# Kernel optimization log

Hardware: AMD Instinct MI355X
Metric: run time of the kernel (lower is better)

Reference implementation:

```python
import jax, jax.numpy as jnp
import numpy as np
from jax import lax

EPSILON = 1e-12


def _sobel_kernels(n1=1, n2=2, n3=2):
    Sx = np.asarray([[[-n1, 0, n1], [-n2, 0, n2], [-n1, 0, n1]],
                     [[-n2, 0, n2], [-n3 * n2, 0, n3 * n2], [-n2, 0, n2]],
                     [[-n1, 0, n1], [-n2, 0, n2], [-n1, 0, n1]]])
    Sy = np.asarray([[[-n1, -n2, -n1], [0, 0, 0], [n1, n2, n1]],
                     [[-n2, -n3 * n2, -n2], [0, 0, 0], [n2, n3 * n2, n2]],
                     [[-n1, -n2, -n1], [0, 0, 0], [n1, n2, n1]]])
    Sz = np.asarray([[[-n1, -n2, -n1], [-n2, -n3 * n2, -n2], [-n1, -n2, -n1]],
                     [[0, 0, 0], [0, 0, 0], [0, 0, 0]],
                     [[n1, n2, n1], [n2, n3 * n2, n2], [n1, n2, n1]]])
    Sd11 = np.asarray([[[0, n1, n2], [-n1, 0, n1], [-n2, -n1, 0]],
                       [[0, n2, n2 * n3], [-n2, 0, n2], [-n2 * n3, -n2, 0]],
                       [[0, n1, n2], [-n1, 0, n1], [-n2, -n1, 0]]])
    Sd12 = np.asarray([[[-n2, -n1, 0], [-n1, 0, n1], [0, n1, n2]],
                       [[-n2 * n3, -n2, 0], [-n2, 0, n2], [0, n2, n2 * n3]],
                       [[-n2, -n1, 0], [-n1, 0, n1], [0, n1, n2]]])
    Sd21 = Sd11.T
    Sd22 = Sd12.T
    Sd31 = np.asarray([-S.T for S in Sd11.T])
    Sd32 = np.asarray([S.T for S in Sd12.T])
    ks = np.stack([Sx, Sy, Sz, Sd11, Sd12, Sd21, Sd22, Sd31, Sd32]).astype(np.float32)
    return jnp.asarray(ks[:, None])  # [9, 1, 3, 3, 3] (OIDHW)


_KERNELS = _sobel_kernels(1, 2, 2)


def _edge_magnitude(img):
    # img: [B, C, H, W, D]. Per-channel convs are summed over C in the original;
    # by linearity of conv, sum channels first, then run all 9 stencils at once.
    C = img.shape[1]
    x = jnp.sum(img, axis=1, keepdims=True)  # [B, 1, H, W, D]
    g = lax.conv_general_dilated(
        x, _KERNELS, window_strides=(1, 1, 1), padding='SAME',
        dimension_numbers=('NCDHW', 'OIDHW', 'NCDHW'))  # [B, 9, H, W, D]
    mag = jnp.sqrt(jnp.sum(g * g, axis=1, keepdims=True) + EPSILON)
    return mag / C  # (1/C) * sqrt(sum_sq + eps), matches operator precedence


def setup_inputs() -> dict:
    key = jax.random.key(0)
    k1, k2 = jax.random.split(key)
    shape = (2, 2, 128, 128, 128)
    y = jax.random.normal(k1, shape, dtype=jnp.float32)
    yp = jax.random.normal(k2, shape, dtype=jnp.float32)
    return {"y": y, "yp": yp}


def reference(y, yp):
    y_edge = _edge_magnitude(y)
    yp_edge = _edge_magnitude(yp)
    return jnp.mean((y_edge - yp_edge) ** 2)  # nn.MSELoss default 'mean'
```

## Files before the change

kernel.cpp:

```cpp
#include <hip/hip_runtime.h>


namespace {

constexpr int ZDIM = 128, YDIM = 128, XDIM = 128;
constexpr int TX = 64, TY = 4, ZC = 16;
constexpr int YX = YDIM * XDIM;
constexpr size_t CS = (size_t)ZDIM * YX;
constexpr float INV_N = 1.0f / 4194304.0f;

__device__ __forceinline__ float bperm(int addr, float v) {
  return __int_as_float(__builtin_amdgcn_ds_bpermute(addr, __float_as_int(v)));
}

__device__ __forceinline__ float edge_mag_half(const float* __restrict__ Ca,
                                               const float* __restrict__ Cb,
                                               const float* __restrict__ Cc) {
  const float g1  = __builtin_fmaf(2.0f, Cb[0], Ca[0] + Cc[0]);
  const float g2  = __builtin_fmaf(2.0f, Cb[1], Ca[1] + Cc[1]);
  const float g3  = Cc[2] - Ca[2];
  const float Azx = __builtin_fmaf(2.0f, Cb[3], Ca[3] + Cc[3]);
  const float Azy = __builtin_fmaf(2.0f, Cb[4], Ca[4] + Cc[4]);
  const float Axz = Cc[5] - Ca[5];
  const float Axy = g2 - Cb[1];
  const float Ayx = g1 - Cb[0];
  const float Ayz = Cc[6] - Ca[6];
  const float g4 = Azx - Azy, g5 = Azx + Azy;
  const float g6 = Axz - Axy, g7 = Axz + Axy;
  const float g8 = Ayx - Ayz, g9 = Ayx + Ayz;
  float s = __builtin_fmaf(g1, g1, 1e-12f);
  s = __builtin_fmaf(g2, g2, s); s = __builtin_fmaf(g3, g3, s);
  s = __builtin_fmaf(g4, g4, s); s = __builtin_fmaf(g5, g5, s);
  s = __builtin_fmaf(g6, g6, s); s = __builtin_fmaf(g7, g7, s);
  s = __builtin_fmaf(g8, g8, s); s = __builtin_fmaf(g9, g9, s);
  return 0.5f * sqrtf(s);
}

__global__ __launch_bounds__(256)
void gme_loss_kernel(const float* __restrict__ y,
                     const float* __restrict__ yp,
                     float* __restrict__ out) {
  const int lane = threadIdx.x;
  const int ty   = threadIdx.y;
  const int tid  = ty * TX + lane;

  const int bx = blockIdx.x;
  const int x0 = (bx & 1) * TX;
  const int yy = (bx >> 1) * TY + ty;
  const int z0 = blockIdx.y * ZC;
  const int b  = blockIdx.z;

  const float* Y0 = y  + (size_t)b * 2 * CS;
  const float* Y1 = Y0 + CS;
  const float* P0 = yp + (size_t)b * 2 * CS;
  const float* P1 = P0 + CS;

  const int vox = yy * XDIM + x0 + lane;
  const bool okM0 = (yy > 0);
  const bool okP0 = (yy < YDIM - 1);

  const bool left  = (lane == 0);
  const bool right = (lane == TX - 1);
  const int  hx    = left ? (x0 - 1) : (x0 + TX);
  const bool hok   = (left && x0 > 0) || (right && x0 + TX < XDIM);
  const int  hxc   = hx < 0 ? 0 : (hx > XDIM - 1 ? XDIM - 1 : hx);
  const int  hvox  = yy * XDIM + hxc;

  const int addrL = (lane > 0 ? lane - 1 : 0) << 2;
  const int addrR = (lane < TX - 1 ? lane + 1 : TX - 1) << 2;

  float pr[2][6];
  float hr[2][6];
  float KY[3][7] = {}, KP[3][7] = {};
  float acc = 0.0f;

  auto loadSum = [&](int buf, int zc) {
    const bool zok = (unsigned)zc < (unsigned)ZDIM;
    const int  zca = zok ? zc : 0;
    const int  o   = zca * YX + vox;
    const int  h   = zca * YX + hvox;
    float ym0=0.f,ym1=0.f,pm0=0.f,pm1=0.f,hym0=0.f,hym1=0.f,hpm0=0.f,hpm1=0.f;
    if (zok && okM0) {
      ym0 = Y0[o - XDIM]; ym1 = Y1[o - XDIM];
      pm0 = P0[o - XDIM]; pm1 = P1[o - XDIM];
      hym0 = Y0[h - XDIM]; hym1 = Y1[h - XDIM];
      hpm0 = P0[h - XDIM]; hpm1 = P1[h - XDIM];
    }
    float yc0=0.f,yc1=0.f,pc0=0.f,pc1=0.f,hyc0=0.f,hyc1=0.f,hpc0=0.f,hpc1=0.f;
    if (zok) {
      yc0 = Y0[o]; yc1 = Y1[o]; pc0 = P0[o]; pc1 = P1[o];
      hyc0 = Y0[h]; hyc1 = Y1[h]; hpc0 = P0[h]; hpc1 = P1[h];
    }
    float yq0=0.f,yq1=0.f,pq0=0.f,pq1=0.f,hyq0=0.f,hyq1=0.f,hpq0=0.f,hpq1=0.f;
    if (zok && okP0) {
      yq0 = Y0[o + XDIM]; yq1 = Y1[o + XDIM];
      pq0 = P0[o + XDIM]; pq1 = P1[o + XDIM];
      hyq0 = Y0[h + XDIM]; hyq1 = Y1[h + XDIM];
      hpq0 = P0[h + XDIM]; hpq1 = P1[h + XDIM];
    }
    pr[buf][0] = ym0 + ym1; pr[buf][1] = yc0 + yc1; pr[buf][2] = yq0 + yq1;
    pr[buf][3] = pm0 + pm1; pr[buf][4] = pc0 + pc1; pr[buf][5] = pq0 + pq1;
    hr[buf][0] = hok ? hym0 + hym1 : 0.f;
    hr[buf][1] = hok ? hyc0 + hyc1 : 0.f;
    hr[buf][2] = hok ? hyq0 + hyq1 : 0.f;
    hr[buf][3] = hok ? hpm0 + hpm1 : 0.f;
    hr[buf][4] = hok ? hpc0 + hpc1 : 0.f;
    hr[buf][5] = hok ? hpq0 + hpq1 : 0.f;
  };

  auto volCombos = [&](float rm, float rc, float rp,
                       float hm, float hc, float hp, float* __restrict__ C) {
    const float t   = rm + rp;
    const float ys  = __builtin_fmaf(2.0f, rc, t);
    const float yd  = rp - rm;
    const float ye  = t + rc;
    const float th  = hm + hp;
    const float hys = __builtin_fmaf(2.0f, hc, th);
    const float hyd = hp - hm;
    const float hye = th + hc;
    float ysL = bperm(addrL, ys), ysR = bperm(addrR, ys);
    float ydL = bperm(addrL, yd), ydR = bperm(addrR, yd);
    float yeL = bperm(addrL, ye), yeR = bperm(addrR, ye);
    ysL = left ? hys : ysL;   ysR = right ? hys : ysR;
    ydL = left ? hyd : ydL;   ydR = right ? hyd : ydR;
    yeL = left ? hye : yeL;   yeR = right ? hye : yeR;
    const float tS = ysL + ysR, tD = ydL + ydR, tE = yeL + yeR;
    C[0] = ysR - ysL;
    C[2] = __builtin_fmaf(2.0f, ys, tS);
    C[6] = tS + ys;
    C[1] = __builtin_fmaf(2.0f, yd, tD);
    C[4] = tD + yd;
    C[3] = yeR - yeL;
    C[5] = __builtin_fmaf(2.0f, ye, tE);
  };

  loadSum(0, z0 - 1);

#pragma unroll 6
  for (int j = 0; j < ZC + 2; ++j) {
    const int cur = j & 1;
    if (j < ZC + 1) loadSum(cur ^ 1, z0 + j);

    float* Cy = KY[j % 3];
    float* Cp = KP[j % 3];
    volCombos(pr[cur][0], pr[cur][1], pr[cur][2],
              hr[cur][0], hr[cur][1], hr[cur][2], Cy);
    volCombos(pr[cur][3], pr[cur][4], pr[cur][5],
              hr[cur][3], hr[cur][4], hr[cur][5], Cp);

    if (j >= 2) {
      const float my = edge_mag_half(KY[(j + 1) % 3], KY[(j + 2) % 3], Cy);
      const float mp = edge_mag_half(KP[(j + 1) % 3], KP[(j + 2) % 3], Cp);
      const float d = my - mp;
      acc = __builtin_fmaf(d, d, acc);
    }
  }

  __shared__ float red[4];
#pragma unroll
  for (int off = 32; off > 0; off >>= 1) acc += __shfl_down(acc, off);
  if (lane == 0) red[ty] = acc;
  __syncthreads();
  if (tid == 0) {
    const float s = (red[0] + red[1] + red[2] + red[3]) * INV_N;
    atomicAdd(out, s);
  }
}

}

extern "C" void kernel_launch(void* const* d_in, const int* in_sizes, int n_in,
                              void* d_out, int out_size, void* d_ws, size_t ws_size,
                              hipStream_t stream) {
  const float* y  = (const float*)d_in[0];
  const float* yp = (const float*)d_in[1];
  float* out = (float*)d_out;

  hipMemsetAsync(out, 0, sizeof(float), stream);

  dim3 block(TX, TY, 1);
  dim3 grid((XDIM / TX) * (YDIM / TY),
            ZDIM / ZC,
            2);
  gme_loss_kernel<<<grid, block, 0, stream>>>(y, yp, out);
}
```

Before: 121.5 us.

## Replace per-edge-lane halo loads with overlapping x tiles

Each wavefront now covers 64 x-positions and produces only the middle 62 outputs, so the x halo comes from neighbouring lanes in the same wave. This removes the divergent extra halo loads (8 extra scalar loads per z-plane) and the halo select logic. The cost is 3 x-tiles instead of 2, which adds about 50% more blocks and redundant loads and compute, and lanes 0 and 63 are masked out of the result. Raw loads are now buffered and the channel sums are deferred into the loop body.

Measured after the change: 117.2 us. 3.5% less time.

```diff
diff --git a/kernel.cpp b/kernel.cpp
--- a/kernel.cpp
+++ b/kernel.cpp
@@ -5,6 +5,8 @@
 
 constexpr int ZDIM = 128, YDIM = 128, XDIM = 128;
 constexpr int TX = 64, TY = 4, ZC = 16;
+constexpr int OTW = 62;
+constexpr int NXT = 3;
 constexpr int YX = YDIM * XDIM;
 constexpr size_t CS = (size_t)ZDIM * YX;
 constexpr float INV_N = 1.0f / 4194304.0f;
@@ -45,8 +47,9 @@
   const int tid  = ty * TX + lane;
 
   const int bx = blockIdx.x;
-  const int x0 = (bx & 1) * TX;
-  const int yy = (bx >> 1) * TY + ty;
+  const int t  = bx % NXT;
+  const int yt = bx / NXT;
+  const int yy = yt * TY + ty;
   const int z0 = blockIdx.y * ZC;
   const int b  = blockIdx.z;
 
@@ -55,75 +58,57 @@
   const float* P0 = yp + (size_t)b * 2 * CS;
   const float* P1 = P0 + CS;
 
-  const int vox = yy * XDIM + x0 + lane;
+  const int  X0  = OTW * t - 1;
+  const int  xg  = X0 + lane;
+  const int  xgc = xg < 0 ? 0 : (xg > XDIM - 1 ? XDIM - 1 : xg);
+  const bool xok = (unsigned)xg < (unsigned)XDIM;
+  const bool eok = xok && (lane >= 1) && (lane <= OTW);
+
+  const int vox = yy * XDIM + xgc;
   const bool okM0 = (yy > 0);
   const bool okP0 = (yy < YDIM - 1);
-
-  const bool left  = (lane == 0);
-  const bool right = (lane == TX - 1);
-  const int  hx    = left ? (x0 - 1) : (x0 + TX);
-  const bool hok   = (left && x0 > 0) || (right && x0 + TX < XDIM);
-  const int  hxc   = hx < 0 ? 0 : (hx > XDIM - 1 ? XDIM - 1 : hx);
-  const int  hvox  = yy * XDIM + hxc;
 
   const int addrL = (lane > 0 ? lane - 1 : 0) << 2;
   const int addrR = (lane < TX - 1 ? lane + 1 : TX - 1) << 2;
 
-  float pr[2][6];
-  float hr[2][6];
+  float pf[2][12];
   float KY[3][7] = {}, KP[3][7] = {};
   float acc = 0.0f;
 
-  auto loadSum = [&](int buf, int zc) {
+  auto loadRaw = [&](int buf, int zc) {
     const bool zok = (unsigned)zc < (unsigned)ZDIM;
     const int  zca = zok ? zc : 0;
     const int  o   = zca * YX + vox;
-    const int  h   = zca * YX + hvox;
-    float ym0=0.f,ym1=0.f,pm0=0.f,pm1=0.f,hym0=0.f,hym1=0.f,hpm0=0.f,hpm1=0.f;
+    float a0=0.f,a1=0.f,a2=0.f,a3=0.f;
     if (zok && okM0) {
-      ym0 = Y0[o - XDIM]; ym1 = Y1[o - XDIM];
-      pm0 = P0[o - XDIM]; pm1 = P1[o - XDIM];
-      hym0 = Y0[h - XDIM]; hym1 = Y1[h - XDIM];
-      hpm0 = P0[h - XDIM]; hpm1 = P1[h - XDIM];
+      a0 = Y0[o - XDIM]; a1 = Y1[o - XDIM];
+      a2 = P0[o - XDIM]; a3 = P1[o - XDIM];
     }
-    float yc0=0.f,yc1=0.f,pc0=0.f,pc1=0.f,hyc0=0.f,hyc1=0.f,hpc0=0.f,hpc1=0.f;
+    float b0=0.f,b1=0.f,b2=0.f,b3=0.f;
     if (zok) {
-      yc0 = Y0[o]; yc1 = Y1[o]; pc0 = P0[o]; pc1 = P1[o];
-      hyc0 = Y0[h]; hyc1 = Y1[h]; hpc0 = P0[h]; hpc1 = P1[h];
+      b0 = Y0[o]; b1 = Y1[o]; b2 = P0[o]; b3 = P1[o];
     }
-    float yq0=0.f,yq1=0.f,pq0=0.f,pq1=0.f,hyq0=0.f,hyq1=0.f,hpq0=0.f,hpq1=0.f;
+    float c0=0.f,c1=0.f,c2=0.f,c3=0.f;
     if (zok && okP0) {
-      yq0 = Y0[o + XDIM]; yq1 = Y1[o + XDIM];
-      pq0 = P0[o + XDIM]; pq1 = P1[o + XDIM];
-      hyq0 = Y0[h + XDIM]; hyq1 = Y1[h + XDIM];
-      hpq0 = P0[h + XDIM]; hpq1 = P1[h + XDIM];
+      c0 = Y0[o + XDIM]; c1 = Y1[o + XDIM];
+      c2 = P0[o + XDIM]; c3 = P1[o + XDIM];
     }
-    pr[buf][0] = ym0 + ym1; pr[buf][1] = yc0 + yc1; pr[buf][2] = yq0 + yq1;
-    pr[buf][3] = pm0 + pm1; pr[buf][4] = pc0 + pc1; pr[buf][5] = pq0 + pq1;
-    hr[buf][0] = hok ? hym0 + hym1 : 0.f;
-    hr[buf][1] = hok ? hyc0 + hyc1 : 0.f;
-    hr[buf][2] = hok ? hyq0 + hyq1 : 0.f;
-    hr[buf][3] = hok ? hpm0 + hpm1 : 0.f;
-    hr[buf][4] = hok ? hpc0 + hpc1 : 0.f;
-    hr[buf][5] = hok ? hpq0 + hpq1 : 0.f;
+    pf[buf][0] = a0;  pf[buf][1] = a1;  pf[buf][2]  = a2;  pf[buf][3]  = a3;
+    pf[buf][4] = b0;  pf[buf][5] = b1;  pf[buf][6]  = b2;  pf[buf][7]  = b3;
+    pf[buf][8] = c0;  pf[buf][9] = c1;  pf[buf][10] = c2;  pf[buf][11] = c3;
   };
 
-  auto volCombos = [&](float rm, float rc, float rp,
-                       float hm, float hc, float hp, float* __restrict__ C) {
-    const float t   = rm + rp;
-    const float ys  = __builtin_fmaf(2.0f, rc, t);
-    const float yd  = rp - rm;
-    const float ye  = t + rc;
-    const float th  = hm + hp;
-    const float hys = __builtin_fmaf(2.0f, hc, th);
-    const float hyd = hp - hm;
-    const float hye = th + hc;
-    float ysL = bperm(addrL, ys), ysR = bperm(addrR, ys);
-    float ydL = bperm(addrL, yd), ydR = bperm(addrR, yd);
-    float yeL = bperm(addrL, ye), yeR = bperm(addrR, ye);
-    ysL = left ? hys : ysL;   ysR = right ? hys : ysR;
-    ydL = left ? hyd : ydL;   ydR = right ? hyd : ydR;
-    yeL = left ? hye : yeL;   yeR = right ? hye : yeR;
+  auto volCombos = [&](float sm, float sc, float sp, float* __restrict__ C) {
+    const float tt = sm + sp;
+    float ys = __builtin_fmaf(2.0f, sc, tt);
+    float yd = sp - sm;
+    float ye = tt + sc;
+    ys = xok ? ys : 0.0f;
+    yd = xok ? yd : 0.0f;
+    ye = xok ? ye : 0.0f;
+    const float ysL = bperm(addrL, ys), ysR = bperm(addrR, ys);
+    const float ydL = bperm(addrL, yd), ydR = bperm(addrR, yd);
+    const float yeL = bperm(addrL, ye), yeR = bperm(addrR, ye);
     const float tS = ysL + ysR, tD = ydL + ydR, tE = yeL + yeR;
     C[0] = ysR - ysL;
     C[2] = __builtin_fmaf(2.0f, ys, tS);
@@ -134,24 +119,28 @@
     C[5] = __builtin_fmaf(2.0f, ye, tE);
   };
 
-  loadSum(0, z0 - 1);
+  loadRaw(0, z0 - 1);
 
 #pragma unroll 6
   for (int j = 0; j < ZC + 2; ++j) {
     const int cur = j & 1;
-    if (j < ZC + 1) loadSum(cur ^ 1, z0 + j);
+    if (j < ZC + 1) loadRaw(cur ^ 1, z0 + j);
+
+    const float* q = pf[cur];
+    const float sYm = q[0] + q[1],  sPm = q[2] + q[3];
+    const float sYc = q[4] + q[5],  sPc = q[6] + q[7];
+    const float sYp = q[8] + q[9],  sPp = q[10] + q[11];
 
     float* Cy = KY[j % 3];
     float* Cp = KP[j % 3];
-    volCombos(pr[cur][0], pr[cur][1], pr[cur][2],
-              hr[cur][0], hr[cur][1], hr[cur][2], Cy);
-    volCombos(pr[cur][3], pr[cur][4], pr[cur][5],
-              hr[cur][3], hr[cur][4], hr[cur][5], Cp);
+    volCombos(sYm, sYc, sYp, Cy);
+    volCombos(sPm, sPc, sPp, Cp);
 
     if (j >= 2) {
       const float my = edge_mag_half(KY[(j + 1) % 3], KY[(j + 2) % 3], Cy);
       const float mp = edge_mag_half(KP[(j + 1) % 3], KP[(j + 2) % 3], Cp);
-      const float d = my - mp;
+      float d = my - mp;
+      d = eok ? d : 0.0f;
       acc = __builtin_fmaf(d, d, acc);
     }
   }
@@ -179,7 +168,7 @@
   hipMemsetAsync(out, 0, sizeof(float), stream);
 
   dim3 block(TX, TY, 1);
-  dim3 grid((XDIM / TX) * (YDIM / TY),
+  dim3 grid(NXT * (YDIM / TY),
             ZDIM / ZC,
             2);
   gme_loss_kernel<<<grid, block, 0, stream>>>(y, yp, out);
```
